# Kernel optimization log

Measured on AMD Instinct MI355X. Metric: run time of the kernel, lower is better.

The kernel has to match this reference:

```python
import jax, jax.numpy as jnp
import numpy as np
from jax import lax

B, C_IN, C_OUT, K, STYLE_DIM, H, W = 8, 512, 512, 3, 512, 64, 64


def setup_inputs() -> dict:
    key = jax.random.key(0)
    k1, k2, k3, k4 = jax.random.split(key, 4)
    return {
        "x": jax.random.normal(k1, (B, C_IN, H, W), dtype=jnp.float32),
        "style": jax.random.normal(k2, (B, STYLE_DIM), dtype=jnp.float32),
        "w": jax.random.normal(k3, (1, C_OUT, C_IN, K, K), dtype=jnp.float32),
        "affine_w": jax.random.normal(k4, (C_IN, STYLE_DIM), dtype=jnp.float32),
        "affine_b": jnp.ones((C_IN,), dtype=jnp.float32),  # bias_init=1
    }


def _per_sample_conv(xi, wi):
    # xi: [C_in, H, W], wi: [C_out, C_in, K, K]; 'same' padding, stride 1
    p = K // 2
    out = lax.conv_general_dilated(
        xi[None], wi, window_strides=(1, 1), padding=[(p, p), (p, p)],
        dimension_numbers=("NCHW", "OIHW", "NCHW"))
    return out[0]


def reference(x, style, w, affine_w, affine_b):
    # Affine (FullyConnected_Layer, linear act, lr_multiplier=1)
    weight_gain_fc = 1.0 / np.sqrt(STYLE_DIM)
    s = style @ (affine_w * weight_gain_fc).T + affine_b  # [B, C_in]

    # Modulate
    weight_gain = 1.0 / np.sqrt(C_IN * K * K)
    weight = w * weight_gain * s[:, None, :, None, None]  # [B, C_out, C_in, K, K]

    # Demodulate
    decoefs = lax.rsqrt(jnp.sum(weight * weight, axis=(2, 3, 4)) + 1e-8)  # [B, C_out]
    weight = weight * decoefs[:, :, None, None, None]

    # Per-sample conv (equivalent to groups=B grouped conv2d)
    out = jax.vmap(_per_sample_conv)(x, weight)  # [B, C_out, H, W]
    return out
```

## Files before the change

### kernel.cpp

```cpp
#include <hip/hip_runtime.h>
#include <hip/hip_bf16.h>


#define CDIM 512
#define HW 64
#define NCHUNK 16
#define XROW 2112

typedef __attribute__((ext_vector_type(8))) short short8;
typedef __attribute__((ext_vector_type(4))) float float4v;

__device__ __forceinline__ short f2bf(float f) {
    unsigned u = __float_as_uint(f);
    unsigned r = (u + 0x7FFFu + ((u >> 16) & 1u)) >> 16;
    return (short)r;
}

__device__ __forceinline__ void async_ld16(const short* g, short* l) {
    __builtin_amdgcn_global_load_lds(
        (const __attribute__((address_space(1))) void*)g,
        (__attribute__((address_space(3))) void*)l, 16, 0, 0);
}

__device__ __forceinline__ void hard_sync() {
    asm volatile("s_waitcnt vmcnt(0) lgkmcnt(0)" ::: "memory");
    __builtin_amdgcn_sched_barrier(0);
    __builtin_amdgcn_s_barrier();
    __builtin_amdgcn_sched_barrier(0);
}


__global__ void k_prep(const float* __restrict__ w, float* __restrict__ ws2,
                       const float* __restrict__ style, const float* __restrict__ aw,
                       const float* __restrict__ ab, float* __restrict__ s) {
    int i = blockIdx.x * 256 + threadIdx.x;
    const float* p = w + i * 9;
    float a = 0.f;
#pragma unroll
    for (int t = 0; t < 9; ++t) a += p[t] * p[t];
    ws2[i] = a;

    int gid = blockIdx.x * 4 + (threadIdx.x >> 6);
    int lane = threadIdx.x & 63;
    int b = gid >> 9, ci = gid & 511;
    const float4v* st = (const float4v*)(style + b * CDIM);
    const float4v* wp = (const float4v*)(aw + ci * CDIM);
    float acc = 0.f;
#pragma unroll
    for (int k = 0; k < 2; ++k) {
        float4v av = st[lane * 2 + k], wv = wp[lane * 2 + k];
        acc += av[0] * wv[0] + av[1] * wv[1] + av[2] * wv[2] + av[3] * wv[3];
    }
#pragma unroll
    for (int off = 32; off; off >>= 1) acc += __shfl_down(acc, off);
    if (lane == 0) s[gid] = acc * 0.04419417382415922f + ab[ci];
}

__global__ void k_oscale(const float* __restrict__ s, const float* __restrict__ ws2,
                         float* __restrict__ osc) {
    int gid = blockIdx.x * 4 + (threadIdx.x >> 6);
    int lane = threadIdx.x & 63;
    int b = gid >> 9, co = gid & 511;
    const float4v* sp = (const float4v*)(s + b * CDIM);
    const float4v* rp = (const float4v*)(ws2 + co * CDIM);
    float acc = 0.f;
#pragma unroll
    for (int k = 0; k < 2; ++k) {
        float4v a = sp[lane * 2 + k], r = rp[lane * 2 + k];
        acc += a[0] * a[0] * r[0] + a[1] * a[1] * r[1]
             + a[2] * a[2] * r[2] + a[3] * a[3] * r[3];
    }
#pragma unroll
    for (int off = 32; off; off >>= 1) acc += __shfl_down(acc, off);
    const float wg = 0.014731391274719739f;
    const float wg2 = 2.170138888888889e-4f;
    if (lane == 0) osc[gid] = wg * rsqrtf(wg2 * acc + 1e-8f);
}

__global__ void k_wconv(const float* __restrict__ w, short* __restrict__ wgt) {
    int idx = blockIdx.x * 256 + threadIdx.x;
    int j = idx & 7;
    int slotg = idx >> 3;
    int region = slotg / 4608;
    int a16 = slotg - region * 4608;
    int tm = a16 >> 6;
    int t = tm >> 3;
    int mf = tm & 7;
    int sl = a16 & 63;
    int l4 = sl >> 4;
    int l15 = sl & 15;
    int ct = region & 3;
    int c = region >> 2;
    int co = ct * 128 + mf * 16 + l15;
    int ci = c * 32 + l4 * 8 + j;
    wgt[idx] = f2bf(w[(co * CDIM + ci) * 9 + t]);
}

__global__ void k_xs(const float* __restrict__ x, const float* __restrict__ s,
                     short* __restrict__ xs, short* __restrict__ zrow) {
    const int bx = blockIdx.x;
    if (bx == 0) {
        short8 z = {};
        for (int u = threadIdx.x; u < 528; u += 256)
            *(short8*)&zrow[u * 8] = z;
    }
    const int grow = bx & 63;
    const int t = bx >> 6;
    const int c = t & 15;
    const int b = t >> 4;
    const int px = threadIdx.x >> 2;
    const int sl = threadIdx.x & 3;
    const int ci0 = c * 32 + sl * 8;
    const float* xb = x + ((b * CDIM + ci0) * HW + grow) * HW + px;
    const float* sb = s + b * CDIM + ci0;
    short8 pk;
#pragma unroll
    for (int j = 0; j < 8; ++j)
        pk[j] = f2bf(xb[j * (HW * HW)] * sb[j]);
    short* rowp = xs + (size_t)bx * XROW;
    *(short8*)&rowp[(px + 1) * 32 + sl * 8] = pk;
    if (threadIdx.x < 8) {
        int col = (threadIdx.x >> 2) ? 65 : 0;
        int s2 = threadIdx.x & 3;
        short8 z = {};
        *(short8*)&rowp[col * 32 + s2 * 8] = z;
    }
}

__global__ __launch_bounds__(512, 1) void conv_main3(
    const short* __restrict__ xs, const short* __restrict__ zrow,
    const short* __restrict__ wgt, const float* __restrict__ osc,
    float* __restrict__ out) {

    __shared__ __align__(16) short w_lds[2][36864];

    const int tid = threadIdx.x;
    const int lane = tid & 63;
    const int wr = tid >> 6;
    const int l15 = lane & 15;
    const int l4 = lane >> 4;

    const int bx = blockIdx.x;
    const int xcd = bx & 7;
    const int t7 = bx >> 3;
    const int ct = t7 & 3;
    const int ghi = t7 >> 2;
    const int b = xcd;
    const int r0 = ghi * 8;

    const int voff = l15 * 32 + l4 * 8;

    auto stage_w = [&](int c, int bufn) {
        const short* src = wgt + (c * 4 + ct) * 36864;
        short* dstb = &w_lds[bufn][0];
#pragma unroll
        for (int k = 0; k < 9; ++k) {
            int off = (k * 512 + wr * 64) * 8;
            async_ld16(src + off + lane * 8, dstb + off + lane * 8);
        }
    };

    float4v acc[8][4] = {};

#define TAPX(T)                                                                  \
    { const short* pd = ((T) < 3) ? p0 : (((T) < 6) ? p1 : p2);                  \
      const int dwp1 = (T) % 3;                                 \
      short8 bfr[4];                                                             \
      _Pragma("unroll")                                                          \
      for (int nf = 0; nf < 4; ++nf)                                             \
          bfr[nf] = *(const short8*)(pd + voff + (nf * 16 + dwp1) * 32);         \
      _Pragma("unroll")                                                          \
      for (int mf = 0; mf < 8; ++mf) {                                           \
          short8 af = *(const short8*)&wb[(((T) * 8 + mf) * 64 + lane) * 8];     \
          _Pragma("unroll")                                                      \
          for (int nf = 0; nf < 4; ++nf)                                         \
              acc[mf][nf] = __builtin_amdgcn_mfma_f32_16x16x32_bf16(             \
                  af, bfr[nf], acc[mf][nf], 0, 0, 0);                            \
      } }

    stage_w(0, 0);
    hard_sync();

    const int gb = r0 + wr - 1;
#pragma unroll 1
    for (int c = 0; c < NCHUNK; ++c) {
        const int buf = c & 1;
        const short* wb = &w_lds[buf][0];
        const short* xcb = xs + ((size_t)(b * 16 + c) * 64) * XROW;
        const short* p0 = ((unsigned)(gb + 0) < 64u) ? xcb + (size_t)(gb + 0) * XROW : zrow;
        const short* p1 = ((unsigned)(gb + 1) < 64u) ? xcb + (size_t)(gb + 1) * XROW : zrow;
        const short* p2 = ((unsigned)(gb + 2) < 64u) ? xcb + (size_t)(gb + 2) * XROW : zrow;

        TAPX(0)
        stage_w((c + 1 < NCHUNK) ? c + 1 : NCHUNK - 1, buf ^ 1);
        __builtin_amdgcn_s_setprio(1);
        TAPX(1) TAPX(2) TAPX(3) TAPX(4)
        TAPX(5) TAPX(6) TAPX(7) TAPX(8)
        __builtin_amdgcn_s_setprio(0);

        asm volatile("s_waitcnt vmcnt(0)" ::: "memory");
        __builtin_amdgcn_sched_barrier(0);
        __builtin_amdgcn_s_barrier();
        __builtin_amdgcn_sched_barrier(0);
    }
#undef TAPX

    const int row_out = r0 + wr;
#pragma unroll
    for (int mf = 0; mf < 8; ++mf) {
        float4v ov = *(const float4v*)&osc[b * CDIM + ct * 128 + mf * 16 + l4 * 4];
#pragma unroll
        for (int j = 0; j < 4; ++j) {
            int co = ct * 128 + mf * 16 + l4 * 4 + j;
            float* po = out + ((b * CDIM + co) * HW + row_out) * HW;
#pragma unroll
            for (int nf = 0; nf < 4; ++nf)
                po[nf * 16 + l15] = acc[mf][nf][j] * ov[j];
        }
    }
}

__global__ __launch_bounds__(512, 1) void conv_main_fb(
    const float* __restrict__ x, const float* __restrict__ s,
    const short* __restrict__ wgt, const float* __restrict__ osc,
    float* __restrict__ out) {

    __shared__ __align__(16) short w_lds[9 * 8 * 64 * 8];
    __shared__ __align__(16) short x_lds[2][10 * 66 * 32];

    const int tid = threadIdx.x;
    const int lane = tid & 63;
    const int wid = tid >> 6;
    const int l15 = lane & 15;
    const int l4 = lane >> 4;

    const int bx = blockIdx.x;
    const int xcd = bx & 7;
    const int t7 = bx >> 3;
    const int ct = t7 & 3;
    const int ghi = t7 >> 2;
    const int b = xcd;
    const int r0 = ghi * 8;

    const int cig = tid & 3;
    const int col = (tid >> 2) & 63;
    const int rowhalf = tid >> 8;

    for (int i = tid; i < 640; i += 512) {
        int bufi = i >= 320;
        int v = i - bufi * 320;
        int row = v >> 5;
        int w16 = v & 31;
        int colh = (w16 >= 16) ? 65 : 0;
        int q16 = w16 & 15;
        ((unsigned*)x_lds[bufi])[(row * 66 + colh) * 16 + q16] = 0u;
    }

    float rx[40];
    float4v sva, svb;

    auto stage_w = [&](int c) {
        const short* src = wgt + (c * 4 + ct) * 36864;
#pragma unroll
        for (int k = 0; k < 9; ++k) {
            int off = (k * 512 + wid * 64) * 8;
            async_ld16(src + off + lane * 8, w_lds + off);
        }
    };

    auto stage_x_load = [&](int c) {
        const float4v* sp = (const float4v*)&s[b * CDIM + c * 32 + cig * 8];
        sva = sp[0]; svb = sp[1];
#pragma unroll
        for (int i = 0; i < 5; ++i) {
            int row = 2 * i + rowhalf;
            int grow = r0 - 1 + row;
            bool ok = (grow >= 0) && (grow < HW);
            const float* base = x + ((b * CDIM + c * 32 + cig * 8) * HW + (ok ? grow : 0)) * HW + col;
#pragma unroll
            for (int j = 0; j < 8; ++j) {
                float v = base[j * (HW * HW)];
                rx[i * 8 + j] = ok ? v : 0.0f;
            }
        }
    };

    auto stage_x_write = [&](int buf) {
        int lcol = col + 1;
        int q = cig ^ ((lcol >> 1) & 3);
#pragma unroll
        for (int i = 0; i < 5; ++i) {
            int row = 2 * i + rowhalf;
            short8 pk;
#pragma unroll
            for (int j = 0; j < 8; ++j) {
                float sj = (j < 4) ? sva[j] : svb[j - 4];
                pk[j] = f2bf(rx[i * 8 + j] * sj);
            }
            *(short8*)&x_lds[buf][(row * 66 + lcol) * 32 + q * 8] = pk;
        }
    };

    float4v acc[8][4] = {};

    auto compute = [&](int buf) {
        const short* xb = x_lds[buf];
#pragma unroll
        for (int t = 0; t < 9; ++t) {
            int dh = t / 3 - 1;
            int dw = t % 3 - 1;
            int lrow = wid + dh + 1;
            short8 bfr[4];
#pragma unroll
            for (int nf = 0; nf < 4; ++nf) {
                int lcol = 1 + nf * 16 + l15 + dw;
                int xq = l4 ^ ((lcol >> 1) & 3);
                bfr[nf] = *(const short8*)&xb[(lrow * 66 + lcol) * 32 + xq * 8];
            }
#pragma unroll
            for (int mf = 0; mf < 8; ++mf) {
                short8 af = *(const short8*)&w_lds[((t * 8 + mf) * 64 + lane) * 8];
#pragma unroll
                for (int nf = 0; nf < 4; ++nf)
                    acc[mf][nf] = __builtin_amdgcn_mfma_f32_16x16x32_bf16(
                        af, bfr[nf], acc[mf][nf], 0, 0, 0);
            }
        }
    };

    stage_w(0);
    stage_x_load(0);
    stage_x_write(0);
    hard_sync();

    int cur = 0;
#pragma unroll 1
    for (int c = 0; c < NCHUNK; ++c) {
        if (c + 1 < NCHUNK) stage_x_load(c + 1);
        compute(cur);
        if (c + 1 < NCHUNK) {
            hard_sync();
            stage_w(c + 1);
            stage_x_write(cur ^ 1);
            hard_sync();
            cur ^= 1;
        }
    }

    const int row_out = r0 + wid;
#pragma unroll
    for (int mf = 0; mf < 8; ++mf) {
        float4v ov = *(const float4v*)&osc[b * CDIM + ct * 128 + mf * 16 + l4 * 4];
#pragma unroll
        for (int j = 0; j < 4; ++j) {
            int co = ct * 128 + mf * 16 + l4 * 4 + j;
            float* po = out + ((b * CDIM + co) * HW + row_out) * HW;
#pragma unroll
            for (int nf = 0; nf < 4; ++nf)
                po[nf * 16 + l15] = acc[mf][nf][j] * ov[j];
        }
    }
}


extern "C" void kernel_launch(void* const* d_in, const int* in_sizes, int n_in,
                              void* d_out, int out_size, void* d_ws, size_t ws_size,
                              hipStream_t stream) {
    const float* x     = (const float*)d_in[0];
    const float* style = (const float*)d_in[1];
    const float* w     = (const float*)d_in[2];
    const float* aw    = (const float*)d_in[3];
    const float* ab    = (const float*)d_in[4];
    float* out = (float*)d_out;

    char* wsb = (char*)d_ws;
    float* s_buf = (float*)(wsb);
    float* ws2   = (float*)(wsb + 16384);
    float* osc   = (float*)(wsb + 1064960);
    short* wgt   = (short*)(wsb + 1081344);
    short* zrow  = (short*)(wsb + 5799936);
    short* xs    = (short*)(wsb + 5804288);
    const size_t need = 5804288ull + 34603008ull;

    k_prep<<<1024, 256, 0, stream>>>(w, ws2, style, aw, ab, s_buf);
    k_wconv<<<9216, 256, 0, stream>>>(w, wgt);
    k_oscale<<<1024, 256, 0, stream>>>(s_buf, ws2, osc);

    if (ws_size >= need) {
        k_xs<<<8192, 256, 0, stream>>>(x, s_buf, xs, zrow);
        conv_main3<<<256, 512, 0, stream>>>(xs, zrow, wgt, osc, out);
    } else {
        conv_main_fb<<<256, 512, 0, stream>>>(x, s_buf, wgt, osc, out);
    }
}
```

Baseline: 152.9 us.

## Split conv blocks into 4-row tiles with single LDS weight buffer, two blocks per CU

```diff
diff --git a/kernel.cpp b/kernel.cpp
--- a/kernel.cpp
+++ b/kernel.cpp
@@ -127,12 +127,12 @@
     }
 }
 
-__global__ __launch_bounds__(512, 1) void conv_main3(
+__global__ __launch_bounds__(256, 2) void conv_main6(
     const short* __restrict__ xs, const short* __restrict__ zrow,
     const short* __restrict__ wgt, const float* __restrict__ osc,
     float* __restrict__ out) {
 
-    __shared__ __align__(16) short w_lds[2][36864];
+    __shared__ __align__(16) short w_lds[36864];
 
     const int tid = threadIdx.x;
     const int lane = tid & 63;
@@ -144,19 +144,18 @@
     const int xcd = bx & 7;
     const int t7 = bx >> 3;
     const int ct = t7 & 3;
-    const int ghi = t7 >> 2;
+    const int rt = t7 >> 2;
     const int b = xcd;
-    const int r0 = ghi * 8;
+    const int r0 = rt * 4;
 
     const int voff = l15 * 32 + l4 * 8;
 
-    auto stage_w = [&](int c, int bufn) {
+    auto stage_w = [&](int c) {
         const short* src = wgt + (c * 4 + ct) * 36864;
-        short* dstb = &w_lds[bufn][0];
-#pragma unroll
-        for (int k = 0; k < 9; ++k) {
-            int off = (k * 512 + wr * 64) * 8;
-            async_ld16(src + off + lane * 8, dstb + off + lane * 8);
+#pragma unroll
+        for (int k = 0; k < 18; ++k) {
+            int u = tid + 256 * k;
+            async_ld16(src + u * 8, w_lds + u * 8);
         }
     };
 
@@ -171,33 +170,36 @@
           bfr[nf] = *(const short8*)(pd + voff + (nf * 16 + dwp1) * 32);         \
       _Pragma("unroll")                                                          \
       for (int mf = 0; mf < 8; ++mf) {                                           \
-          short8 af = *(const short8*)&wb[(((T) * 8 + mf) * 64 + lane) * 8];     \
+          short8 af = *(const short8*)&w_lds[(((T) * 8 + mf) * 64 + lane) * 8];  \
           _Pragma("unroll")                                                      \
           for (int nf = 0; nf < 4; ++nf)                                         \
               acc[mf][nf] = __builtin_amdgcn_mfma_f32_16x16x32_bf16(             \
                   af, bfr[nf], acc[mf][nf], 0, 0, 0);                            \
       } }
 
-    stage_w(0, 0);
+    stage_w(0);
     hard_sync();
 
     const int gb = r0 + wr - 1;
 #pragma unroll 1
     for (int c = 0; c < NCHUNK; ++c) {
-        const int buf = c & 1;
-        const short* wb = &w_lds[buf][0];
         const short* xcb = xs + ((size_t)(b * 16 + c) * 64) * XROW;
         const short* p0 = ((unsigned)(gb + 0) < 64u) ? xcb + (size_t)(gb + 0) * XROW : zrow;
         const short* p1 = ((unsigned)(gb + 1) < 64u) ? xcb + (size_t)(gb + 1) * XROW : zrow;
         const short* p2 = ((unsigned)(gb + 2) < 64u) ? xcb + (size_t)(gb + 2) * XROW : zrow;
 
-        TAPX(0)
-        stage_w((c + 1 < NCHUNK) ? c + 1 : NCHUNK - 1, buf ^ 1);
         __builtin_amdgcn_s_setprio(1);
-        TAPX(1) TAPX(2) TAPX(3) TAPX(4)
+        TAPX(0) TAPX(1) TAPX(2) TAPX(3) TAPX(4)
         TAPX(5) TAPX(6) TAPX(7) TAPX(8)
         __builtin_amdgcn_s_setprio(0);
 
+        __builtin_amdgcn_sched_barrier(0);
+        asm volatile("s_waitcnt lgkmcnt(0)" ::: "memory");
+        __builtin_amdgcn_s_barrier();
+        __builtin_amdgcn_sched_barrier(0);
+
+        stage_w((c + 1 < NCHUNK) ? c + 1 : NCHUNK - 1);
+        __builtin_amdgcn_sched_barrier(0);
         asm volatile("s_waitcnt vmcnt(0)" ::: "memory");
         __builtin_amdgcn_sched_barrier(0);
         __builtin_amdgcn_s_barrier();
@@ -388,7 +390,7 @@
 
     if (ws_size >= need) {
         k_xs<<<8192, 256, 0, stream>>>(x, s_buf, xs, zrow);
-        conv_main3<<<256, 512, 0, stream>>>(xs, zrow, wgt, osc, out);
+        conv_main6<<<512, 256, 0, stream>>>(xs, zrow, wgt, osc, out);
     } else {
         conv_main_fb<<<256, 512, 0, stream>>>(x, s_buf, wgt, osc, out);
     }
```

Result: slower. 158.7 us (+3.8%).
